# Kernel optimization log

Measured on AMD Instinct MI355X. Metric: run time of the kernel, lower is better.

Reference implementation:

```python
import jax, jax.numpy as jnp
import numpy as np

N = 100000
E = 1600000
HID = 128
EPS = 1e-8


def _linear_params(key, fan_in, fan_out, bias=True, gain=1.0):
    kw, kb = jax.random.split(key)
    bound = gain / np.sqrt(fan_in)
    W = jax.random.uniform(kw, (fan_in, fan_out), jnp.float32, -bound, bound)
    if bias:
        b = jax.random.uniform(kb, (fan_out,), jnp.float32, -bound, bound)
        return W, b
    return W


def setup_inputs() -> dict:
    key = jax.random.key(0)
    ks = jax.random.split(key, 12)
    h = jax.random.normal(ks[0], (N, HID), jnp.float32)
    coord = jax.random.normal(ks[1], (N, 3), jnp.float32)
    edge_index = jax.random.randint(ks[2], (2, E), 0, N, jnp.int64)
    # edge_mlp: Linear(2*HID+1 -> HID), SiLU, Linear(HID -> HID), SiLU
    We1, be1 = _linear_params(ks[3], 2 * HID + 1, HID)
    We2, be2 = _linear_params(ks[4], HID, HID)
    # node_mlp: Linear(2*HID -> HID), SiLU, Linear(HID -> HID)
    Wn1, bn1 = _linear_params(ks[5], 2 * HID, HID)
    Wn2, bn2 = _linear_params(ks[6], HID, HID)
    # coord_mlp: Linear(HID -> HID), SiLU, Linear(HID -> 1, no bias, xavier gain=0.001)
    Wc1, bc1 = _linear_params(ks[7], HID, HID)
    Wc2 = _linear_params(ks[8], HID, 1, bias=False, gain=0.001 * np.sqrt(6.0 * HID / (HID + 1)))
    return {
        "h": h, "edge_index": edge_index, "coord": coord,
        "We1": We1, "be1": be1, "We2": We2, "be2": be2,
        "Wn1": Wn1, "bn1": bn1, "Wn2": Wn2, "bn2": bn2,
        "Wc1": Wc1, "bc1": bc1, "Wc2": Wc2,
    }


def _egcl(h, edge_index, coord, We1, be1, We2, be2, Wn1, bn1, Wn2, bn2, Wc1, bc1, Wc2):
    row, col = edge_index[0], edge_index[1]
    n = h.shape[0]
    # coord2radial (normalize=True, detach on norm)
    coord_diff = coord[row] - coord[col]                       # [E,3]
    radial = jnp.sum(coord_diff ** 2, axis=1, keepdims=True)   # [E,1]
    norm = jax.lax.stop_gradient(jnp.sqrt(radial)) + EPS
    coord_diff = coord_diff / norm
    # edge_model (no edge_attr, no attention)
    edge_in = jnp.concatenate([h[row], h[col], radial], axis=1)  # [E, 2H+1]
    m = jax.nn.silu(edge_in @ We1 + be1)
    m = jax.nn.silu(m @ We2 + be2)                               # [E,H]
    # coord_model (coords_agg='mean', tanh=False)
    phi_x = jax.nn.silu(m @ Wc1 + bc1) @ Wc2                     # [E,1]
    trans = coord_diff * phi_x                                   # [E,3]
    agg_c = jax.ops.segment_sum(trans, row, num_segments=n)
    cnt = jax.ops.segment_sum(jnp.ones((trans.shape[0],), trans.dtype), row, num_segments=n)
    agg_c = agg_c / jnp.clip(cnt, 1.0, None)[:, None]
    coord_out = coord + agg_c
    # node_model (residual=True)
    agg_h = jax.ops.segment_sum(m, row, num_segments=n)          # [N,H]
    node_in = jnp.concatenate([h, agg_h], axis=1)
    out = jax.nn.silu(node_in @ Wn1 + bn1) @ Wn2 + bn2
    h_out = h + out
    return h_out, coord_out


def reference(h, edge_index, coord, We1, be1, We2, be2, Wn1, bn1, Wn2, bn2, Wc1, bc1, Wc2):
    return _egcl(h, edge_index, coord, We1, be1, We2, be2, Wn1, bn1, Wn2, bn2, Wc1, bc1, Wc2)
```

## Files before the change

kernel.cpp:

```cpp
#include <hip/hip_runtime.h>

#define NN 100000
#define NE 1600000
#define HD 128
#define EPSV 1e-8f
#define EB 64
#define LPAD 136

typedef unsigned short ushort_t;
typedef __attribute__((ext_vector_type(8))) short bf16x8;
typedef __attribute__((ext_vector_type(4))) float f32x4;

__device__ __forceinline__ float silu_f(float x) {
    return x * __builtin_amdgcn_rcpf(1.0f + __expf(-x));
}
__device__ __forceinline__ float b2f(unsigned short u) {
    union { unsigned int i; float f; } v; v.i = ((unsigned int)u) << 16; return v.f;
}
__device__ __forceinline__ unsigned short f2b(float f) {
    union { float f; unsigned int i; } v; v.f = f;
    unsigned int r = v.i + 0x7fff + ((v.i >> 16) & 1);
    return (unsigned short)(r >> 16);
}
__device__ __forceinline__ unsigned int cvt_pk_bf16(float lo, float hi) {
    unsigned int r;
    asm("v_cvt_pk_bf16_f32 %0, %1, %2" : "=v"(r) : "v"(lo), "v"(hi));
    return r;
}
__device__ __forceinline__ bf16x8 frag_from_f32(const float* p) {
    float4 a0 = *(const float4*)p;
    float4 a1 = *(const float4*)(p + 4);
    union { bf16x8 v; uint4 u; } r;
    r.u.x = cvt_pk_bf16(a0.x, a0.y); r.u.y = cvt_pk_bf16(a0.z, a0.w);
    r.u.z = cvt_pk_bf16(a1.x, a1.y); r.u.w = cvt_pk_bf16(a1.z, a1.w);
    return r.v;
}

extern "C" __global__ __launch_bounds__(256)
void k_prep_hist(const int* __restrict__ ei, int* __restrict__ deg,
                 const float* __restrict__ We2, const float* __restrict__ Wc1,
                 const float* __restrict__ We1, const float* __restrict__ Wn1,
                 const float* __restrict__ Wn2,
                 ushort_t* __restrict__ We2T, ushort_t* __restrict__ Wc1T,
                 ushort_t* __restrict__ WabT, ushort_t* __restrict__ Wn1T,
                 ushort_t* __restrict__ Wn2T)
{
    int id = blockIdx.x * 256 + threadIdx.x;
    atomicAdd(&deg[ei[id]], 1);
    if (id < 16384) {
        int n = id >> 7, k = id & 127;
        We2T[id] = f2b(We2[k * HD + n]);
    } else if (id < 32768) {
        int r = id - 16384; int n = r >> 7, k = r & 127;
        Wc1T[r] = f2b(Wc1[k * HD + n]);
    } else if (id < 65536) {
        int r = id - 32768; int j = r >> 7, k = r & 127;
        float v = (j < 128) ? We1[k * HD + j] : We1[(size_t)(128 + k) * HD + (j - 128)];
        WabT[r] = f2b(v);
    } else if (id < 98304) {
        int r = id - 65536; int j = r >> 8, k = r & 255;
        Wn1T[r] = f2b(Wn1[(size_t)k * HD + j]);
    } else if (id < 114688) {
        int r = id - 98304; int j = r >> 7, k = r & 127;
        Wn2T[r] = f2b(Wn2[k * HD + j]);
    }
}

extern "C" __global__ __launch_bounds__(1024)
void k_scan1(const int* __restrict__ deg, int* __restrict__ bsum)
{
    __shared__ int wsum[16];
    const int tid = threadIdx.x;
    const int lane = tid & 63, w = tid >> 6;
    int i = blockIdx.x * 1024 + tid;
    int v = (i < NN) ? deg[i] : 0;
#pragma unroll
    for (int off = 32; off > 0; off >>= 1) v += __shfl_xor(v, off, 64);
    if (lane == 0) wsum[w] = v;
    __syncthreads();
    if (tid == 0) {
        int s = 0;
#pragma unroll
        for (int k = 0; k < 16; k++) s += wsum[k];
        bsum[blockIdx.x] = s;
    }
}

extern "C" __global__ __launch_bounds__(1024)
void k_scan3(const int* __restrict__ deg, const int* __restrict__ bsum,
             int* __restrict__ cursor)
{
    __shared__ int wsum[16];
    __shared__ int boff_s;
    const int tid = threadIdx.x;
    const int lane = tid & 63, w = tid >> 6;
    int i = blockIdx.x * 1024 + tid;
    int v = (i < NN) ? deg[i] : 0;
    int s = v;
#pragma unroll
    for (int off = 1; off < 64; off <<= 1) {
        int t = __shfl_up(s, off, 64);
        if (lane >= off) s += t;
    }
    if (lane == 63) wsum[w] = s;
    if (w == 0) {
        int a = 0;
        for (int k = lane; k < blockIdx.x; k += 64) a += bsum[k];
#pragma unroll
        for (int off = 32; off > 0; off >>= 1) a += __shfl_xor(a, off, 64);
        if (lane == 0) boff_s = a;
    }
    __syncthreads();
    if (w == 0) {
        int ws = (lane < 16) ? wsum[lane] : 0;
#pragma unroll
        for (int off = 1; off < 16; off <<= 1) {
            int t = __shfl_up(ws, off, 64);
            if (lane >= off) ws += t;
        }
        if (lane < 16) wsum[lane] = ws;
    }
    __syncthreads();
    int excl = boff_s + ((w > 0) ? wsum[w - 1] : 0) + s - v;
    if (i < NN) cursor[i] = excl;
}

extern "C" __global__ __launch_bounds__(256)
void k_sortids(const int* __restrict__ ei, int* __restrict__ cursor,
               int2* __restrict__ rc)
{
    int e = blockIdx.x * 256 + threadIdx.x;
    int r = ei[e], c = ei[NE + e];
    int slot = atomicAdd(&cursor[r], 1);
    rc[slot] = make_int2(r, c);
}

extern "C" __global__ __launch_bounds__(256)
void k_ab(const float* __restrict__ h, const ushort_t* __restrict__ WabT,
          const float* __restrict__ be1,
          ushort_t* __restrict__ A, ushort_t* __restrict__ B)
{
    const int tid = threadIdx.x;
    const int n0 = blockIdx.x * 64;
    const int wave = tid >> 6, lane = tid & 63;
    const int lr = lane & 15, lg = lane >> 4;
    const int node = n0 + wave * 16 + lr;
    const int nsrc = (node < NN) ? node : (NN - 1);

    f32x4 acc[16];
#pragma unroll
    for (int nt = 0; nt < 16; nt++) acc[nt] = (f32x4){0.f, 0.f, 0.f, 0.f};
#pragma unroll
    for (int ks = 0; ks < 4; ks++) {
        bf16x8 hf8 = frag_from_f32(h + (size_t)nsrc * HD + ks * 32 + lg * 8);
#pragma unroll
        for (int nt = 0; nt < 16; nt++) {
            bf16x8 wf = *(const bf16x8*)(WabT + (size_t)(nt * 16 + lr) * HD + ks * 32 + lg * 8);
            acc[nt] = __builtin_amdgcn_mfma_f32_16x16x32_bf16(wf, hf8, acc[nt], 0, 0, 0);
        }
    }
    if (node < NN) {
#pragma unroll
        for (int nt = 0; nt < 16; nt++) {
            float4 bias = (nt < 8) ? ((const float4*)be1)[nt * 4 + lg]
                                   : (float4){0.f, 0.f, 0.f, 0.f};
            uint2 pk;
            pk.x = cvt_pk_bf16(acc[nt][0] + bias.x, acc[nt][1] + bias.y);
            pk.y = cvt_pk_bf16(acc[nt][2] + bias.z, acc[nt][3] + bias.w);
            if (nt < 8)
                *(uint2*)(A + (size_t)node * HD + nt * 16 + lg * 4) = pk;
            else
                *(uint2*)(B + (size_t)node * HD + (nt - 8) * 16 + lg * 4) = pk;
        }
    }
}

extern "C" __global__ __launch_bounds__(128, 4)
void k_edge(const int2* __restrict__ rc, const float* __restrict__ coord,
            const ushort_t* __restrict__ A, const ushort_t* __restrict__ B,
            const float* __restrict__ WeL, const float* __restrict__ be2,
            const ushort_t* __restrict__ We2T,
            const ushort_t* __restrict__ Wc1T,
            const float* __restrict__ bc1, const float* __restrict__ Wc2,
            float* __restrict__ agg_h, float* __restrict__ agg_c)
{
    __shared__ ushort_t m_lds[EB][LPAD] __attribute__((aligned(16)));
    __shared__ float cd_lds[EB][3];
    __shared__ int rows_s[EB];
    __shared__ float bias_lds[384] __attribute__((aligned(16)));
    __shared__ float wel_lds[128] __attribute__((aligned(16)));

    const int tid = threadIdx.x;
    const int e  = tid >> 1;
    const int hf = tid & 1;
    const int wave = tid >> 6, lane = tid & 63;
    const int lr = lane & 15, lg = lane >> 4;

    {
        int i = tid;
        bias_lds[i]       = be2[i];
        bias_lds[128 + i] = bc1[i];
        bias_lds[256 + i] = Wc2[i];
        wel_lds[i] = WeL[i];
    }
    int2 rce = rc[blockIdx.x * EB + e];
    const int row = rce.x, col = rce.y;

    float c0 = coord[(size_t)row * 3 + 0] - coord[(size_t)col * 3 + 0];
    float c1 = coord[(size_t)row * 3 + 1] - coord[(size_t)col * 3 + 1];
    float c2 = coord[(size_t)row * 3 + 2] - coord[(size_t)col * 3 + 2];
    float radial = c0 * c0 + c1 * c1 + c2 * c2;
    if (hf == 0) {
        rows_s[e] = row;
        float inv = __builtin_amdgcn_rcpf(sqrtf(radial) + EPSV);
        cd_lds[e][0] = c0 * inv; cd_lds[e][1] = c1 * inv; cd_lds[e][2] = c2 * inv;
    }
    __syncthreads();

    {
        const bf16x8* A8 = (const bf16x8*)(A + (size_t)row * HD + hf * 64);
        const bf16x8* B8 = (const bf16x8*)(B + (size_t)col * HD + hf * 64);
        const float4* WL4 = (const float4*)wel_lds + hf * 16;
#pragma unroll
        for (int i = 0; i < 8; i++) {
            bf16x8 av = A8[i], bv = B8[i];
            float4 w0 = WL4[2 * i], w1 = WL4[2 * i + 1];
            float v0 = silu_f(b2f((ushort_t)av[0]) + b2f((ushort_t)bv[0]) + radial * w0.x);
            float v1 = silu_f(b2f((ushort_t)av[1]) + b2f((ushort_t)bv[1]) + radial * w0.y);
            float v2 = silu_f(b2f((ushort_t)av[2]) + b2f((ushort_t)bv[2]) + radial * w0.z);
            float v3 = silu_f(b2f((ushort_t)av[3]) + b2f((ushort_t)bv[3]) + radial * w0.w);
            float v4 = silu_f(b2f((ushort_t)av[4]) + b2f((ushort_t)bv[4]) + radial * w1.x);
            float v5 = silu_f(b2f((ushort_t)av[5]) + b2f((ushort_t)bv[5]) + radial * w1.y);
            float v6 = silu_f(b2f((ushort_t)av[6]) + b2f((ushort_t)bv[6]) + radial * w1.z);
            float v7 = silu_f(b2f((ushort_t)av[7]) + b2f((ushort_t)bv[7]) + radial * w1.w);
            uint4 p;
            p.x = cvt_pk_bf16(v0, v1); p.y = cvt_pk_bf16(v2, v3);
            p.z = cvt_pk_bf16(v4, v5); p.w = cvt_pk_bf16(v6, v7);
            *(uint4*)&m_lds[e][hf * 64 + i * 8] = p;
        }
    }

    f32x4 acc[2][8];
#pragma unroll
    for (int mt = 0; mt < 2; mt++)
#pragma unroll
        for (int nt = 0; nt < 8; nt++) acc[mt][nt] = (f32x4){0.f, 0.f, 0.f, 0.f};
#pragma unroll
    for (int ks = 0; ks < 4; ks++) {
        bf16x8 mf0 = *(const bf16x8*)&m_lds[wave * 32 + lr][ks * 32 + lg * 8];
        bf16x8 mf1 = *(const bf16x8*)&m_lds[wave * 32 + 16 + lr][ks * 32 + lg * 8];
#pragma unroll
        for (int nt = 0; nt < 8; nt++) {
            bf16x8 wf = *(const bf16x8*)(We2T + (size_t)(nt * 16 + lr) * HD + ks * 32 + lg * 8);
            acc[0][nt] = __builtin_amdgcn_mfma_f32_16x16x32_bf16(wf, mf0, acc[0][nt], 0, 0, 0);
            acc[1][nt] = __builtin_amdgcn_mfma_f32_16x16x32_bf16(wf, mf1, acc[1][nt], 0, 0, 0);
        }
    }
#pragma unroll
    for (int nt = 0; nt < 8; nt++) {
        float4 be2v = *(const float4*)&bias_lds[nt * 16 + lg * 4];
#pragma unroll
        for (int mt = 0; mt < 2; mt++) {
            float v0 = silu_f(acc[mt][nt][0] + be2v.x);
            float v1 = silu_f(acc[mt][nt][1] + be2v.y);
            float v2 = silu_f(acc[mt][nt][2] + be2v.z);
            float v3 = silu_f(acc[mt][nt][3] + be2v.w);
            uint2 pk; pk.x = cvt_pk_bf16(v0, v1); pk.y = cvt_pk_bf16(v2, v3);
            *(uint2*)&m_lds[wave * 32 + mt * 16 + lr][nt * 16 + lg * 4] = pk;
        }
    }

#pragma unroll
    for (int mt = 0; mt < 2; mt++)
#pragma unroll
        for (int nt = 0; nt < 8; nt++) acc[mt][nt] = (f32x4){0.f, 0.f, 0.f, 0.f};
#pragma unroll
    for (int ks = 0; ks < 4; ks++) {
        bf16x8 mf0 = *(const bf16x8*)&m_lds[wave * 32 + lr][ks * 32 + lg * 8];
        bf16x8 mf1 = *(const bf16x8*)&m_lds[wave * 32 + 16 + lr][ks * 32 + lg * 8];
#pragma unroll
        for (int nt = 0; nt < 8; nt++) {
            bf16x8 wf = *(const bf16x8*)(Wc1T + (size_t)(nt * 16 + lr) * HD + ks * 32 + lg * 8);
            acc[0][nt] = __builtin_amdgcn_mfma_f32_16x16x32_bf16(wf, mf0, acc[0][nt], 0, 0, 0);
            acc[1][nt] = __builtin_amdgcn_mfma_f32_16x16x32_bf16(wf, mf1, acc[1][nt], 0, 0, 0);
        }
    }

    float ph0 = 0.f, ph1 = 0.f;
#pragma unroll
    for (int nt = 0; nt < 8; nt++) {
        float4 bc1v = *(const float4*)&bias_lds[128 + nt * 16 + lg * 4];
        float4 wc2v = *(const float4*)&bias_lds[256 + nt * 16 + lg * 4];
        ph0 += silu_f(acc[0][nt][0] + bc1v.x) * wc2v.x
             + silu_f(acc[0][nt][1] + bc1v.y) * wc2v.y
             + silu_f(acc[0][nt][2] + bc1v.z) * wc2v.z
             + silu_f(acc[0][nt][3] + bc1v.w) * wc2v.w;
        ph1 += silu_f(acc[1][nt][0] + bc1v.x) * wc2v.x
             + silu_f(acc[1][nt][1] + bc1v.y) * wc2v.y
             + silu_f(acc[1][nt][2] + bc1v.z) * wc2v.z
             + silu_f(acc[1][nt][3] + bc1v.w) * wc2v.w;
    }
    ph0 += __shfl_xor(ph0, 16, 64); ph0 += __shfl_xor(ph0, 32, 64);
    ph1 += __shfl_xor(ph1, 16, 64); ph1 += __shfl_xor(ph1, 32, 64);
    if (lg == 0) {
        int e0 = wave * 32 + lr, e1 = e0 + 16;
        cd_lds[e0][0] *= ph0; cd_lds[e0][1] *= ph0; cd_lds[e0][2] *= ph0;
        cd_lds[e1][0] *= ph1; cd_lds[e1][1] *= ph1; cd_lds[e1][2] *= ph1;
    }

    __syncthreads();

    {
        const int j = tid;
        float acc_r = 0.f;
        int cur = rows_s[0];
        for (int es = 0; es < EB; es++) {
            int r = rows_s[es];
            if (r != cur) {
                atomicAdd(&agg_h[(size_t)cur * HD + j], acc_r);
                acc_r = 0.f; cur = r;
            }
            acc_r += b2f(m_lds[es][j]);
        }
        atomicAdd(&agg_h[(size_t)cur * HD + j], acc_r);
    }
    if (wave == 0) {
        int c = lane >> 4, sub = lane & 15;
        if (c < 3) {
            const int es0 = sub * 4, es1 = es0 + 4;
            float acc_r = 0.f;
            int cur = rows_s[es0];
            for (int es = es0; es < es1; es++) {
                int r = rows_s[es];
                if (r != cur) {
                    atomicAdd(&agg_c[(size_t)cur * 3 + c], acc_r);
                    acc_r = 0.f; cur = r;
                }
                acc_r += cd_lds[es][c];
            }
            atomicAdd(&agg_c[(size_t)cur * 3 + c], acc_r);
        }
    }
}

extern "C" __global__ __launch_bounds__(256)
void k_node(const float* __restrict__ h, const ushort_t* __restrict__ Wn1T,
            const float* __restrict__ bn1, const ushort_t* __restrict__ Wn2T,
            const float* __restrict__ bn2, const float* __restrict__ coord,
            const int* __restrict__ deg,
            float* __restrict__ hout ,
            float* __restrict__ cout )
{
    __shared__ ushort_t us[64][LPAD] __attribute__((aligned(16)));
    const int tid = threadIdx.x;
    const int n0 = blockIdx.x * 64;
    const int wave = tid >> 6, lane = tid & 63;
    const int lr = lane & 15, lg = lane >> 4;
    const int node = n0 + wave * 16 + lr;
    const int nsrc = (node < NN) ? node : (NN - 1);

    f32x4 acc[8];
#pragma unroll
    for (int nt = 0; nt < 8; nt++) acc[nt] = (f32x4){0.f, 0.f, 0.f, 0.f};
#pragma unroll
    for (int ks = 0; ks < 8; ks++) {
        const float* src = (ks < 4) ? (h + (size_t)nsrc * HD + ks * 32 + lg * 8)
                                    : (hout + (size_t)nsrc * HD + (ks - 4) * 32 + lg * 8);
        bf16x8 cf = frag_from_f32(src);
#pragma unroll
        for (int nt = 0; nt < 8; nt++) {
            bf16x8 wf = *(const bf16x8*)(Wn1T + (size_t)(nt * 16 + lr) * 256 + ks * 32 + lg * 8);
            acc[nt] = __builtin_amdgcn_mfma_f32_16x16x32_bf16(wf, cf, acc[nt], 0, 0, 0);
        }
    }
#pragma unroll
    for (int nt = 0; nt < 8; nt++) {
        float4 b1 = ((const float4*)bn1)[nt * 4 + lg];
        float v0 = silu_f(acc[nt][0] + b1.x);
        float v1 = silu_f(acc[nt][1] + b1.y);
        float v2 = silu_f(acc[nt][2] + b1.z);
        float v3 = silu_f(acc[nt][3] + b1.w);
        uint2 pk; pk.x = cvt_pk_bf16(v0, v1); pk.y = cvt_pk_bf16(v2, v3);
        *(uint2*)&us[wave * 16 + lr][nt * 16 + lg * 4] = pk;
    }

    f32x4 acc2[8];
#pragma unroll
    for (int nt = 0; nt < 8; nt++) acc2[nt] = (f32x4){0.f, 0.f, 0.f, 0.f};
#pragma unroll
    for (int ks = 0; ks < 4; ks++) {
        bf16x8 uf = *(const bf16x8*)&us[wave * 16 + lr][ks * 32 + lg * 8];
#pragma unroll
        for (int nt = 0; nt < 8; nt++) {
            bf16x8 wf = *(const bf16x8*)(Wn2T + (size_t)(nt * 16 + lr) * HD + ks * 32 + lg * 8);
            acc2[nt] = __builtin_amdgcn_mfma_f32_16x16x32_bf16(wf, uf, acc2[nt], 0, 0, 0);
        }
    }
    if (node < NN) {
#pragma unroll
        for (int nt = 0; nt < 8; nt++) {
            float4 b2 = ((const float4*)bn2)[nt * 4 + lg];
            size_t idx = (size_t)node * HD + nt * 16 + lg * 4;
            float4 hv = *(const float4*)(h + idx);
            float4 o;
            o.x = hv.x + acc2[nt][0] + b2.x;
            o.y = hv.y + acc2[nt][1] + b2.y;
            o.z = hv.z + acc2[nt][2] + b2.z;
            o.w = hv.w + acc2[nt][3] + b2.w;
            *(float4*)(hout + idx) = o;
        }
        if (lg == 0) {
            float invc = __builtin_amdgcn_rcpf(fmaxf((float)deg[node], 1.0f));
#pragma unroll
            for (int i = 0; i < 3; i++) {
                size_t idx = (size_t)node * 3 + i;
                cout[idx] = coord[idx] + cout[idx] * invc;
            }
        }
    }
}

extern "C" void kernel_launch(void* const* d_in, const int* in_sizes, int n_in,
                              void* d_out, int out_size, void* d_ws, size_t ws_size,
                              hipStream_t stream)
{
    const float* h     = (const float*)d_in[0];
    const int*   ei    = (const int*)d_in[1];
    const float* coord = (const float*)d_in[2];
    const float* We1   = (const float*)d_in[3];
    const float* be1   = (const float*)d_in[4];
    const float* We2   = (const float*)d_in[5];
    const float* be2   = (const float*)d_in[6];
    const float* Wn1   = (const float*)d_in[7];
    const float* bn1   = (const float*)d_in[8];
    const float* Wn2   = (const float*)d_in[9];
    const float* bn2   = (const float*)d_in[10];
    const float* Wc1   = (const float*)d_in[11];
    const float* bc1   = (const float*)d_in[12];
    const float* Wc2   = (const float*)d_in[13];

    float* out   = (float*)d_out;
    float* agg_h = out;
    float* agg_c = out + (size_t)NN * HD;

    ushort_t* A    = (ushort_t*)d_ws;
    ushort_t* B    = A + (size_t)NN * HD;
    ushort_t* We2T = B + (size_t)NN * HD;
    ushort_t* Wc1T = We2T + 16384;
    ushort_t* WabT = Wc1T + 16384;
    ushort_t* Wn1T = WabT + 32768;
    ushort_t* Wn2T = Wn1T + 32768;
    int* deg    = (int*)(Wn2T + 16384);
    int* cursor = deg + NN;
    int* bsum   = cursor + NN;
    int2* rc    = (int2*)(bsum + 128);
    const float* WeL = We1 + (size_t)2 * HD * HD;

    const int scan_nb = (NN + 1023) / 1024;

    hipMemsetAsync(d_out, 0, (size_t)out_size * sizeof(float), stream);
    hipMemsetAsync(deg, 0, (size_t)NN * sizeof(int), stream);

    k_prep_hist<<<NE / 256, 256, 0, stream>>>(ei, deg, We2, Wc1, We1, Wn1, Wn2,
                                              We2T, Wc1T, WabT, Wn1T, Wn2T);
    k_ab<<<(NN + 63) / 64, 256, 0, stream>>>(h, WabT, be1, A, B);
    k_scan1<<<scan_nb, 1024, 0, stream>>>(deg, bsum);
    k_scan3<<<scan_nb, 1024, 0, stream>>>(deg, bsum, cursor);
    k_sortids<<<NE / 256, 256, 0, stream>>>(ei, cursor, rc);
    k_edge<<<NE / EB, 128, 0, stream>>>(rc, coord, A, B, WeL, be2,
                                        We2T, Wc1T, bc1, Wc2, agg_h, agg_c);
    k_node<<<(NN + 63) / 64, 256, 0, stream>>>(h, Wn1T, bn1, Wn2T, bn2, coord,
                                               deg, agg_h, agg_c);
}
```

Measured before the change: 882.1 us.

## Process two edge tiles per block with prefetch of next tile's gathers

Each edge block now handles two 64-edge tiles in sequence. While the first tile runs its MFMA layers, the block prefetches the next tile's indices, coordinates and B-row gather into registers, hiding gather latency behind compute. Block count halves, bias loads are amortised, and the launch-bounds occupancy hint is dropped. The cost is higher register pressure from the prefetched B rows, which may reduce occupancy.

Result: slower. 1.221 ms (+38.4%).

```diff
diff --git a/kernel.cpp b/kernel.cpp
--- a/kernel.cpp
+++ b/kernel.cpp
@@ -175,7 +175,7 @@
     }
 }
 
-extern "C" __global__ __launch_bounds__(128, 4)
+extern "C" __global__ __launch_bounds__(128)
 void k_edge(const int2* __restrict__ rc, const float* __restrict__ coord,
             const ushort_t* __restrict__ A, const ushort_t* __restrict__ B,
             const float* __restrict__ WeL, const float* __restrict__ be2,
@@ -196,149 +196,183 @@
     const int wave = tid >> 6, lane = tid & 63;
     const int lr = lane & 15, lg = lane >> 4;
 
+    bias_lds[tid]       = be2[tid];
+    bias_lds[128 + tid] = bc1[tid];
+    bias_lds[256 + tid] = Wc2[tid];
+    wel_lds[tid] = WeL[tid];
+
+    const size_t base = (size_t)blockIdx.x * (2 * EB);
+
+    int2 rce = rc[base + e];
+    int row = rce.x, col = rce.y;
+    float crx = coord[(size_t)row * 3 + 0], cry = coord[(size_t)row * 3 + 1],
+          crz = coord[(size_t)row * 3 + 2];
+    float ccx = coord[(size_t)col * 3 + 0], ccy = coord[(size_t)col * 3 + 1],
+          ccz = coord[(size_t)col * 3 + 2];
+    bf16x8 Bst[8];
     {
-        int i = tid;
-        bias_lds[i]       = be2[i];
-        bias_lds[128 + i] = bc1[i];
-        bias_lds[256 + i] = Wc2[i];
-        wel_lds[i] = WeL[i];
-    }
-    int2 rce = rc[blockIdx.x * EB + e];
-    const int row = rce.x, col = rce.y;
-
-    float c0 = coord[(size_t)row * 3 + 0] - coord[(size_t)col * 3 + 0];
-    float c1 = coord[(size_t)row * 3 + 1] - coord[(size_t)col * 3 + 1];
-    float c2 = coord[(size_t)row * 3 + 2] - coord[(size_t)col * 3 + 2];
-    float radial = c0 * c0 + c1 * c1 + c2 * c2;
-    if (hf == 0) {
-        rows_s[e] = row;
-        float inv = __builtin_amdgcn_rcpf(sqrtf(radial) + EPSV);
-        cd_lds[e][0] = c0 * inv; cd_lds[e][1] = c1 * inv; cd_lds[e][2] = c2 * inv;
-    }
+        const bf16x8* Bp = (const bf16x8*)(B + (size_t)col * HD + hf * 64);
+#pragma unroll
+        for (int i = 0; i < 8; i++) Bst[i] = Bp[i];
+    }
+
     __syncthreads();
 
-    {
-        const bf16x8* A8 = (const bf16x8*)(A + (size_t)row * HD + hf * 64);
-        const bf16x8* B8 = (const bf16x8*)(B + (size_t)col * HD + hf * 64);
-        const float4* WL4 = (const float4*)wel_lds + hf * 16;
-#pragma unroll
-        for (int i = 0; i < 8; i++) {
-            bf16x8 av = A8[i], bv = B8[i];
-            float4 w0 = WL4[2 * i], w1 = WL4[2 * i + 1];
-            float v0 = silu_f(b2f((ushort_t)av[0]) + b2f((ushort_t)bv[0]) + radial * w0.x);
-            float v1 = silu_f(b2f((ushort_t)av[1]) + b2f((ushort_t)bv[1]) + radial * w0.y);
-            float v2 = silu_f(b2f((ushort_t)av[2]) + b2f((ushort_t)bv[2]) + radial * w0.z);
-            float v3 = silu_f(b2f((ushort_t)av[3]) + b2f((ushort_t)bv[3]) + radial * w0.w);
-            float v4 = silu_f(b2f((ushort_t)av[4]) + b2f((ushort_t)bv[4]) + radial * w1.x);
-            float v5 = silu_f(b2f((ushort_t)av[5]) + b2f((ushort_t)bv[5]) + radial * w1.y);
-            float v6 = silu_f(b2f((ushort_t)av[6]) + b2f((ushort_t)bv[6]) + radial * w1.z);
-            float v7 = silu_f(b2f((ushort_t)av[7]) + b2f((ushort_t)bv[7]) + radial * w1.w);
-            uint4 p;
-            p.x = cvt_pk_bf16(v0, v1); p.y = cvt_pk_bf16(v2, v3);
-            p.z = cvt_pk_bf16(v4, v5); p.w = cvt_pk_bf16(v6, v7);
-            *(uint4*)&m_lds[e][hf * 64 + i * 8] = p;
-        }
-    }
-
-    f32x4 acc[2][8];
-#pragma unroll
-    for (int mt = 0; mt < 2; mt++)
-#pragma unroll
-        for (int nt = 0; nt < 8; nt++) acc[mt][nt] = (f32x4){0.f, 0.f, 0.f, 0.f};
-#pragma unroll
-    for (int ks = 0; ks < 4; ks++) {
-        bf16x8 mf0 = *(const bf16x8*)&m_lds[wave * 32 + lr][ks * 32 + lg * 8];
-        bf16x8 mf1 = *(const bf16x8*)&m_lds[wave * 32 + 16 + lr][ks * 32 + lg * 8];
+#pragma unroll
+    for (int t = 0; t < 2; t++) {
+        float c0 = crx - ccx, c1 = cry - ccy, c2 = crz - ccz;
+        float radial = c0 * c0 + c1 * c1 + c2 * c2;
+        if (hf == 0) {
+            rows_s[e] = row;
+            float inv = __builtin_amdgcn_rcpf(sqrtf(radial) + EPSV);
+            cd_lds[e][0] = c0 * inv; cd_lds[e][1] = c1 * inv; cd_lds[e][2] = c2 * inv;
+        }
+
+        {
+            const bf16x8* A8 = (const bf16x8*)(A + (size_t)row * HD + hf * 64);
+            const float4* WL4 = (const float4*)wel_lds + hf * 16;
+#pragma unroll
+            for (int i = 0; i < 8; i++) {
+                bf16x8 av = A8[i], bv = Bst[i];
+                float4 w0 = WL4[2 * i], w1 = WL4[2 * i + 1];
+                float v0 = silu_f(b2f((ushort_t)av[0]) + b2f((ushort_t)bv[0]) + radial * w0.x);
+                float v1 = silu_f(b2f((ushort_t)av[1]) + b2f((ushort_t)bv[1]) + radial * w0.y);
+                float v2 = silu_f(b2f((ushort_t)av[2]) + b2f((ushort_t)bv[2]) + radial * w0.z);
+                float v3 = silu_f(b2f((ushort_t)av[3]) + b2f((ushort_t)bv[3]) + radial * w0.w);
+                float v4 = silu_f(b2f((ushort_t)av[4]) + b2f((ushort_t)bv[4]) + radial * w1.x);
+                float v5 = silu_f(b2f((ushort_t)av[5]) + b2f((ushort_t)bv[5]) + radial * w1.y);
+                float v6 = silu_f(b2f((ushort_t)av[6]) + b2f((ushort_t)bv[6]) + radial * w1.z);
+                float v7 = silu_f(b2f((ushort_t)av[7]) + b2f((ushort_t)bv[7]) + radial * w1.w);
+                uint4 p;
+                p.x = cvt_pk_bf16(v0, v1); p.y = cvt_pk_bf16(v2, v3);
+                p.z = cvt_pk_bf16(v4, v5); p.w = cvt_pk_bf16(v6, v7);
+                *(uint4*)&m_lds[e][hf * 64 + i * 8] = p;
+            }
+        }
+
+        int nrow = row;
+        float ncrx = crx, ncry = cry, ncrz = crz;
+        float nccx = ccx, nccy = ccy, nccz = ccz;
+        if (t == 0) {
+            int2 rcn = rc[base + EB + e];
+            nrow = rcn.x;
+            int ncol = rcn.y;
+            ncrx = coord[(size_t)nrow * 3 + 0]; ncry = coord[(size_t)nrow * 3 + 1];
+            ncrz = coord[(size_t)nrow * 3 + 2];
+            nccx = coord[(size_t)ncol * 3 + 0]; nccy = coord[(size_t)ncol * 3 + 1];
+            nccz = coord[(size_t)ncol * 3 + 2];
+            const bf16x8* Bp = (const bf16x8*)(B + (size_t)ncol * HD + hf * 64);
+#pragma unroll
+            for (int i = 0; i < 8; i++) Bst[i] = Bp[i];
+        }
+
+        f32x4 acc[2][8];
+#pragma unroll
+        for (int mt = 0; mt < 2; mt++)
+#pragma unroll
+            for (int nt = 0; nt < 8; nt++) acc[mt][nt] = (f32x4){0.f, 0.f, 0.f, 0.f};
+#pragma unroll
+        for (int ks = 0; ks < 4; ks++) {
+            bf16x8 mf0 = *(const bf16x8*)&m_lds[wave * 32 + lr][ks * 32 + lg * 8];
+            bf16x8 mf1 = *(const bf16x8*)&m_lds[wave * 32 + 16 + lr][ks * 32 + lg * 8];
+#pragma unroll
+            for (int nt = 0; nt < 8; nt++) {
+                bf16x8 wf = *(const bf16x8*)(We2T + (size_t)(nt * 16 + lr) * HD + ks * 32 + lg * 8);
+                acc[0][nt] = __builtin_amdgcn_mfma_f32_16x16x32_bf16(wf, mf0, acc[0][nt], 0, 0, 0);
+                acc[1][nt] = __builtin_amdgcn_mfma_f32_16x16x32_bf16(wf, mf1, acc[1][nt], 0, 0, 0);
+            }
+        }
 #pragma unroll
         for (int nt = 0; nt < 8; nt++) {
-            bf16x8 wf = *(const bf16x8*)(We2T + (size_t)(nt * 16 + lr) * HD + ks * 32 + lg * 8);
-            acc[0][nt] = __builtin_amdgcn_mfma_f32_16x16x32_bf16(wf, mf0, acc[0][nt], 0, 0, 0);
-            acc[1][nt] = __builtin_amdgcn_mfma_f32_16x16x32_bf16(wf, mf1, acc[1][nt], 0, 0, 0);
-        }
-    }
-#pragma unroll
-    for (int nt = 0; nt < 8; nt++) {
-        float4 be2v = *(const float4*)&bias_lds[nt * 16 + lg * 4];
-#pragma unroll
-        for (int mt = 0; mt < 2; mt++) {
-            float v0 = silu_f(acc[mt][nt][0] + be2v.x);
-            float v1 = silu_f(acc[mt][nt][1] + be2v.y);
-            float v2 = silu_f(acc[mt][nt][2] + be2v.z);
-            float v3 = silu_f(acc[mt][nt][3] + be2v.w);
-            uint2 pk; pk.x = cvt_pk_bf16(v0, v1); pk.y = cvt_pk_bf16(v2, v3);
-            *(uint2*)&m_lds[wave * 32 + mt * 16 + lr][nt * 16 + lg * 4] = pk;
-        }
-    }
-
-#pragma unroll
-    for (int mt = 0; mt < 2; mt++)
-#pragma unroll
-        for (int nt = 0; nt < 8; nt++) acc[mt][nt] = (f32x4){0.f, 0.f, 0.f, 0.f};
-#pragma unroll
-    for (int ks = 0; ks < 4; ks++) {
-        bf16x8 mf0 = *(const bf16x8*)&m_lds[wave * 32 + lr][ks * 32 + lg * 8];
-        bf16x8 mf1 = *(const bf16x8*)&m_lds[wave * 32 + 16 + lr][ks * 32 + lg * 8];
+            float4 be2v = *(const float4*)&bias_lds[nt * 16 + lg * 4];
+#pragma unroll
+            for (int mt = 0; mt < 2; mt++) {
+                float v0 = silu_f(acc[mt][nt][0] + be2v.x);
+                float v1 = silu_f(acc[mt][nt][1] + be2v.y);
+                float v2 = silu_f(acc[mt][nt][2] + be2v.z);
+                float v3 = silu_f(acc[mt][nt][3] + be2v.w);
+                uint2 pk; pk.x = cvt_pk_bf16(v0, v1); pk.y = cvt_pk_bf16(v2, v3);
+                *(uint2*)&m_lds[wave * 32 + mt * 16 + lr][nt * 16 + lg * 4] = pk;
+            }
+        }
+
+#pragma unroll
+        for (int mt = 0; mt < 2; mt++)
+#pragma unroll
+            for (int nt = 0; nt < 8; nt++) acc[mt][nt] = (f32x4){0.f, 0.f, 0.f, 0.f};
+#pragma unroll
+        for (int ks = 0; ks < 4; ks++) {
+            bf16x8 mf0 = *(const bf16x8*)&m_lds[wave * 32 + lr][ks * 32 + lg * 8];
+            bf16x8 mf1 = *(const bf16x8*)&m_lds[wave * 32 + 16 + lr][ks * 32 + lg * 8];
+#pragma unroll
+            for (int nt = 0; nt < 8; nt++) {
+                bf16x8 wf = *(const bf16x8*)(Wc1T + (size_t)(nt * 16 + lr) * HD + ks * 32 + lg * 8);
+                acc[0][nt] = __builtin_amdgcn_mfma_f32_16x16x32_bf16(wf, mf0, acc[0][nt], 0, 0, 0);
+                acc[1][nt] = __builtin_amdgcn_mfma_f32_16x16x32_bf16(wf, mf1, acc[1][nt], 0, 0, 0);
+            }
+        }
+
+        float ph0 = 0.f, ph1 = 0.f;
 #pragma unroll
         for (int nt = 0; nt < 8; nt++) {
-            bf16x8 wf = *(const bf16x8*)(Wc1T + (size_t)(nt * 16 + lr) * HD + ks * 32 + lg * 8);
-            acc[0][nt] = __builtin_amdgcn_mfma_f32_16x16x32_bf16(wf, mf0, acc[0][nt], 0, 0, 0);
-            acc[1][nt] = __builtin_amdgcn_mfma_f32_16x16x32_bf16(wf, mf1, acc[1][nt], 0, 0, 0);
-        }
-    }
-
-    float ph0 = 0.f, ph1 = 0.f;
-#pragma unroll
-    for (int nt = 0; nt < 8; nt++) {
-        float4 bc1v = *(const float4*)&bias_lds[128 + nt * 16 + lg * 4];
-        float4 wc2v = *(const float4*)&bias_lds[256 + nt * 16 + lg * 4];
-        ph0 += silu_f(acc[0][nt][0] + bc1v.x) * wc2v.x
-             + silu_f(acc[0][nt][1] + bc1v.y) * wc2v.y
-             + silu_f(acc[0][nt][2] + bc1v.z) * wc2v.z
-             + silu_f(acc[0][nt][3] + bc1v.w) * wc2v.w;
-        ph1 += silu_f(acc[1][nt][0] + bc1v.x) * wc2v.x
-             + silu_f(acc[1][nt][1] + bc1v.y) * wc2v.y
-             + silu_f(acc[1][nt][2] + bc1v.z) * wc2v.z
-             + silu_f(acc[1][nt][3] + bc1v.w) * wc2v.w;
-    }
-    ph0 += __shfl_xor(ph0, 16, 64); ph0 += __shfl_xor(ph0, 32, 64);
-    ph1 += __shfl_xor(ph1, 16, 64); ph1 += __shfl_xor(ph1, 32, 64);
-    if (lg == 0) {
-        int e0 = wave * 32 + lr, e1 = e0 + 16;
-        cd_lds[e0][0] *= ph0; cd_lds[e0][1] *= ph0; cd_lds[e0][2] *= ph0;
-        cd_lds[e1][0] *= ph1; cd_lds[e1][1] *= ph1; cd_lds[e1][2] *= ph1;
-    }
-
-    __syncthreads();
-
-    {
-        const int j = tid;
-        float acc_r = 0.f;
-        int cur = rows_s[0];
-        for (int es = 0; es < EB; es++) {
-            int r = rows_s[es];
-            if (r != cur) {
-                atomicAdd(&agg_h[(size_t)cur * HD + j], acc_r);
-                acc_r = 0.f; cur = r;
-            }
-            acc_r += b2f(m_lds[es][j]);
-        }
-        atomicAdd(&agg_h[(size_t)cur * HD + j], acc_r);
-    }
-    if (wave == 0) {
-        int c = lane >> 4, sub = lane & 15;
-        if (c < 3) {
-            const int es0 = sub * 4, es1 = es0 + 4;
+            float4 bc1v = *(const float4*)&bias_lds[128 + nt * 16 + lg * 4];
+            float4 wc2v = *(const float4*)&bias_lds[256 + nt * 16 + lg * 4];
+            ph0 += silu_f(acc[0][nt][0] + bc1v.x) * wc2v.x
+                 + silu_f(acc[0][nt][1] + bc1v.y) * wc2v.y
+                 + silu_f(acc[0][nt][2] + bc1v.z) * wc2v.z
+                 + silu_f(acc[0][nt][3] + bc1v.w) * wc2v.w;
+            ph1 += silu_f(acc[1][nt][0] + bc1v.x) * wc2v.x
+                 + silu_f(acc[1][nt][1] + bc1v.y) * wc2v.y
+                 + silu_f(acc[1][nt][2] + bc1v.z) * wc2v.z
+                 + silu_f(acc[1][nt][3] + bc1v.w) * wc2v.w;
+        }
+        ph0 += __shfl_xor(ph0, 16, 64); ph0 += __shfl_xor(ph0, 32, 64);
+        ph1 += __shfl_xor(ph1, 16, 64); ph1 += __shfl_xor(ph1, 32, 64);
+        if (lg == 0) {
+            int e0 = wave * 32 + lr, e1 = e0 + 16;
+            cd_lds[e0][0] *= ph0; cd_lds[e0][1] *= ph0; cd_lds[e0][2] *= ph0;
+            cd_lds[e1][0] *= ph1; cd_lds[e1][1] *= ph1; cd_lds[e1][2] *= ph1;
+        }
+
+        __syncthreads();
+
+        {
+            const int j = tid;
             float acc_r = 0.f;
-            int cur = rows_s[es0];
-            for (int es = es0; es < es1; es++) {
+            int cur = rows_s[0];
+            for (int es = 0; es < EB; es++) {
                 int r = rows_s[es];
                 if (r != cur) {
-                    atomicAdd(&agg_c[(size_t)cur * 3 + c], acc_r);
+                    atomicAdd(&agg_h[(size_t)cur * HD + j], acc_r);
                     acc_r = 0.f; cur = r;
                 }
-                acc_r += cd_lds[es][c];
-            }
-            atomicAdd(&agg_c[(size_t)cur * 3 + c], acc_r);
+                acc_r += b2f(m_lds[es][j]);
+            }
+            atomicAdd(&agg_h[(size_t)cur * HD + j], acc_r);
+        }
+        if (wave == 0) {
+            int c = lane >> 4, sub = lane & 15;
+            if (c < 3) {
+                const int es0 = sub * 4, es1 = es0 + 4;
+                float acc_r = 0.f;
+                int cur = rows_s[es0];
+                for (int es = es0; es < es1; es++) {
+                    int r = rows_s[es];
+                    if (r != cur) {
+                        atomicAdd(&agg_c[(size_t)cur * 3 + c], acc_r);
+                        acc_r = 0.f; cur = r;
+                    }
+                    acc_r += cd_lds[es][c];
+                }
+                atomicAdd(&agg_c[(size_t)cur * 3 + c], acc_r);
+            }
+        }
+
+        if (t == 0) {
+            row = nrow;
+            crx = ncrx; cry = ncry; crz = ncrz;
+            ccx = nccx; ccy = nccy; ccz = nccz;
+            __syncthreads();
         }
     }
 }
@@ -467,8 +501,8 @@
     k_scan1<<<scan_nb, 1024, 0, stream>>>(deg, bsum);
     k_scan3<<<scan_nb, 1024, 0, stream>>>(deg, bsum, cursor);
     k_sortids<<<NE / 256, 256, 0, stream>>>(ei, cursor, rc);
-    k_edge<<<NE / EB, 128, 0, stream>>>(rc, coord, A, B, WeL, be2,
-                                        We2T, Wc1T, bc1, Wc2, agg_h, agg_c);
+    k_edge<<<NE / (2 * EB), 128, 0, stream>>>(rc, coord, A, B, WeL, be2,
+                                              We2T, Wc1T, bc1, Wc2, agg_h, agg_c);
     k_node<<<(NN + 63) / 64, 256, 0, stream>>>(h, Wn1T, bn1, Wn2T, bn2, coord,
                                                deg, agg_h, agg_c);
 }
```
